# Kernel optimization log

Hardware: AMD Instinct MI355X
Metric: run time of the kernel (lower is better)

## Reference

```python
import jax, jax.numpy as jnp
import numpy as np

B, DIM, HEADS, HEAD_DIM = 4, 768, 8, 96
THW = (8, 28, 28)
N_TOK = THW[0] * THW[1] * THW[2] + 1  # +1 cls token = 6273
HIDDEN = 4 * DIM
STRIDE = (1, 2, 2)
SCALE = HEAD_DIM ** -0.5


def layernorm(x, w, b, eps=1e-5):
    mu = x.mean(-1, keepdims=True)
    var = ((x - mu) ** 2).mean(-1, keepdims=True)
    return (x - mu) / jnp.sqrt(var + eps) * w + b


def conv_pool(x, w):
    # depthwise 3D conv: x [BN, C, T, H, W], w [C, 1, 3, 3, 3], stride (1,2,2), pad 1
    return jax.lax.conv_general_dilated(
        x, w, window_strides=STRIDE, padding=[(1, 1), (1, 1), (1, 1)],
        dimension_numbers=('NCDHW', 'OIDHW', 'NCDHW'),
        feature_group_count=x.shape[1])


def attn_pool(x, conv_w, norm_w, norm_b):
    # x: [B, h, N, d]; pool spatial tokens (excluding cls), then LayerNorm(head_dim)
    cls, xs = x[:, :, :1], x[:, :, 1:]
    b, h, _, d = xs.shape
    t, hh, ww = THW
    xs = xs.reshape(b * h, t, hh, ww, d).transpose(0, 4, 1, 2, 3)  # [bh, d, t, h, w]
    xs = conv_pool(xs, conv_w)
    l_pooled = xs.shape[2] * xs.shape[3] * xs.shape[4]
    xs = xs.reshape(b, h, d, l_pooled).transpose(0, 1, 3, 2)  # [B, h, L, d]
    xs = jnp.concatenate([cls, xs], axis=2)
    return layernorm(xs, norm_w, norm_b)


def max_pool_skip(x):
    # residual-path MaxPool3d: kernel (1,3,3), stride (1,2,2), pad (0,1,1); cls excluded
    cls, xs = x[:, :1], x[:, 1:]
    b, _, c = xs.shape
    t, hh, ww = THW
    xs = xs.reshape(b, t, hh, ww, c)
    xs = jax.lax.reduce_window(
        xs, -jnp.inf, jax.lax.max,
        (1, 1, 3, 3, 1), (1, 1, 2, 2, 1),
        [(0, 0), (0, 0), (1, 1), (1, 1), (0, 0)])
    xs = xs.reshape(b, -1, c)
    return jnp.concatenate([cls, xs], axis=1)


def setup_inputs() -> dict:
    key = jax.random.key(0)
    ks = jax.random.split(key, 16)
    s = 0.02
    inp = {
        'x': jax.random.normal(ks[0], (B, N_TOK, DIM), jnp.float32),
        'n1_w': jnp.ones((DIM,), jnp.float32), 'n1_b': jnp.zeros((DIM,), jnp.float32),
        'wq': jax.random.normal(ks[1], (DIM, DIM), jnp.float32) * s,
        'bq': jnp.zeros((DIM,), jnp.float32),
        'wk': jax.random.normal(ks[2], (DIM, DIM), jnp.float32) * s,
        'bk': jnp.zeros((DIM,), jnp.float32),
        'wv': jax.random.normal(ks[3], (DIM, DIM), jnp.float32) * s,
        'bv': jnp.zeros((DIM,), jnp.float32),
        'pq_w': jax.random.normal(ks[4], (HEAD_DIM, 1, 3, 3, 3), jnp.float32) * s,
        'pk_w': jax.random.normal(ks[5], (HEAD_DIM, 1, 3, 3, 3), jnp.float32) * s,
        'pv_w': jax.random.normal(ks[6], (HEAD_DIM, 1, 3, 3, 3), jnp.float32) * s,
        'nq_w': jnp.ones((HEAD_DIM,), jnp.float32), 'nq_b': jnp.zeros((HEAD_DIM,), jnp.float32),
        'nk_w': jnp.ones((HEAD_DIM,), jnp.float32), 'nk_b': jnp.zeros((HEAD_DIM,), jnp.float32),
        'nv_w': jnp.ones((HEAD_DIM,), jnp.float32), 'nv_b': jnp.zeros((HEAD_DIM,), jnp.float32),
        'proj_w': jax.random.normal(ks[7], (DIM, DIM), jnp.float32) * s,
        'proj_b': jnp.zeros((DIM,), jnp.float32),
        'n2_w': jnp.ones((DIM,), jnp.float32), 'n2_b': jnp.zeros((DIM,), jnp.float32),
        'fc1_w': jax.random.normal(ks[8], (HIDDEN, DIM), jnp.float32) * s,
        'fc1_b': jnp.zeros((HIDDEN,), jnp.float32),
        'fc2_w': jax.random.normal(ks[9], (DIM, HIDDEN), jnp.float32) * s,
        'fc2_b': jnp.zeros((DIM,), jnp.float32),
    }
    return inp


def reference(x, n1_w, n1_b, wq, bq, wk, bk, wv, bv, pq_w, pk_w, pv_w,
              nq_w, nq_b, nk_w, nk_b, nv_w, nv_b, proj_w, proj_b,
              n2_w, n2_b, fc1_w, fc1_b, fc2_w, fc2_b):
    b, n, _ = x.shape
    xn = layernorm(x, n1_w, n1_b)
    # q/k/v projections -> [B, h, N, d]
    q = (xn @ wq.T + bq).reshape(b, n, HEADS, HEAD_DIM).transpose(0, 2, 1, 3)
    k = (xn @ wk.T + bk).reshape(b, n, HEADS, HEAD_DIM).transpose(0, 2, 1, 3)
    v = (xn @ wv.T + bv).reshape(b, n, HEADS, HEAD_DIM).transpose(0, 2, 1, 3)
    q = attn_pool(q, pq_w, nq_w, nq_b)
    k = attn_pool(k, pk_w, nk_w, nk_b)
    v = attn_pool(v, pv_w, nv_w, nv_b)
    attn = jax.nn.softmax(jnp.einsum('bhqd,bhkd->bhqk', q, k) * SCALE, axis=-1)
    o = jnp.einsum('bhqk,bhkd->bhqd', attn, v)
    nq = o.shape[2]
    o = o.transpose(0, 2, 1, 3).reshape(b, nq, DIM)
    o = o @ proj_w.T + proj_b
    # residual with pooled skip
    x2 = max_pool_skip(x) + o
    xn2 = layernorm(x2, n2_w, n2_b)
    m = jax.nn.gelu(xn2 @ fc1_w.T + fc1_b, approximate=False) @ fc2_w.T + fc2_b
    return x2 + m
```

## Files before the change

kernel.cpp:

```cpp
#include <hip/hip_runtime.h>
#include <math.h>

#define B_ 4
#define NTOK 6273
#define DIMD 768
#define HEADS 8
#define HD 96
#define NPOOL 1569
#define NPAD 1600
#define HID 3072
#define MROWS (B_*NTOK)
#define M2 (B_*NPOOL)
#define SCALE_ 0.10206207261596575f

typedef float f32x4 __attribute__((ext_vector_type(4)));
typedef short s16x8 __attribute__((ext_vector_type(8)));
typedef short s16x4 __attribute__((ext_vector_type(4)));
typedef unsigned u32x3 __attribute__((ext_vector_type(3)));

__device__ __forceinline__ short f2bf(float f){
  unsigned u = __builtin_bit_cast(unsigned, f);
  u = (u + 0x7fffu + ((u >> 16) & 1u)) >> 16;
  return (short)u;
}
__device__ __forceinline__ float bf2f(short s){
  unsigned u = ((unsigned)(unsigned short)s) << 16;
  return __builtin_bit_cast(float, u);
}
__device__ __forceinline__ float bfsel(unsigned u, int hi){
  unsigned r = hi ? (u & 0xffff0000u) : (u << 16);
  return __builtin_bit_cast(float, r);
}
__device__ __forceinline__ unsigned pack2(float lo, float hi){
  return (unsigned)(unsigned short)f2bf(lo) | ((unsigned)(unsigned short)f2bf(hi) << 16);
}

__device__ __forceinline__ void gld16(const void* g, void* l){
  __builtin_amdgcn_global_load_lds((const __attribute__((address_space(1))) unsigned*)g,
                                   (__attribute__((address_space(3))) unsigned*)l, 16, 0, 0);
}

#if defined(__has_builtin)
#if __has_builtin(__builtin_amdgcn_mfma_f32_16x16x16bf16_1k)
#define MFMA16K(a,b,c) __builtin_amdgcn_mfma_f32_16x16x16bf16_1k(a,b,c,0,0,0)
#endif
#endif
#ifndef MFMA16K
__device__ __forceinline__ f32x4 mfma16k_asm(s16x4 a, s16x4 b, f32x4 c){
  asm volatile("v_mfma_f32_16x16x16_bf16 %0, %1, %2, %0\n\ts_nop 7\n\ts_nop 7"
               : "+v"(c) : "v"(a), "v"(b));
  return c;
}
#define MFMA16K(a,b,c) mfma16k_asm(a,b,c)
#endif

template<int NT>
__device__ __forceinline__ float block_sum(float v, float* red){
  int t = threadIdx.x;
  red[t] = v; __syncthreads();
  #pragma unroll
  for (int s = NT/2; s > 0; s >>= 1){
    if (t < s) red[t] += red[t+s];
    __syncthreads();
  }
  float r = red[0];
  __syncthreads();
  return r;
}

__device__ __forceinline__ unsigned xcd_serial(unsigned bid, unsigned nwg){
  unsigned q = nwg >> 3, r8 = nwg & 7;
  unsigned xcd = bid & 7, idx = bid >> 3;
  return (xcd < r8 ? xcd*(q+1) : r8*(q+1) + (xcd-r8)*q) + idx;
}

template<int STR, int STC>
__device__ __forceinline__ void tile_decode(unsigned serial, int& rowT, int& colT){
  const int nStC = (int)gridDim.x / STC;
  int st = (int)serial / (STR*STC);
  int t  = (int)serial - st*(STR*STC);
  int stR = st / nStC, stC = st - stR*nStC;
  int c = t / STR, r = t - c*STR;
  rowT = stR*STR + r;
  colT = stC*STC + c;
}

__global__ void castw(const float* s0,const float* s1,const float* s2,const float* s3,
                      const float* s4,const float* s5,
                      short* d0,short* d1,short* d2,short* d3,short* d4,short* d5){
  const float* s; short* d; int n;
  switch(blockIdx.y){
    case 0: s=s0; d=d0; n=589824; break;
    case 1: s=s1; d=d1; n=589824; break;
    case 2: s=s2; d=d2; n=589824; break;
    case 3: s=s3; d=d3; n=589824; break;
    case 4: s=s4; d=d4; n=2359296; break;
    default: s=s5; d=d5; n=2359296; break;
  }
  for (int i = blockIdx.x*blockDim.x + threadIdx.x; i < n; i += gridDim.x*blockDim.x)
    d[i] = f2bf(s[i]);
}

__global__ __launch_bounds__(256) void packb(const float* b0, const float* b1, const float* b2, float* o){
  int i = blockIdx.x*256 + threadIdx.x;
  if (i < 768) o[i] = b0[i];
  else if (i < 1536) o[i] = b1[i-768];
  else if (i < 2304) o[i] = b2[i-1536];
}

__global__ __launch_bounds__(256) void ln768(const float* __restrict__ x, const float* __restrict__ w,
                      const float* __restrict__ b, short* __restrict__ out){
  int row = blockIdx.x*4 + (threadIdx.x >> 6);
  int lane = threadIdx.x & 63;
  const float* xr = x + (size_t)row*DIMD + lane*12;
  f32x4 v0 = *(const f32x4*)(xr);
  f32x4 v1 = *(const f32x4*)(xr + 4);
  f32x4 v2 = *(const f32x4*)(xr + 8);
  float v[12] = { v0[0],v0[1],v0[2],v0[3], v1[0],v1[1],v1[2],v1[3], v2[0],v2[1],v2[2],v2[3] };
  float s = 0.f;
  #pragma unroll
  for (int j=0;j<12;j++) s += v[j];
  #pragma unroll
  for (int m=1; m<64; m<<=1) s += __shfl_xor(s, m);
  float mu = s * (1.f/768.f);
  float sq = 0.f;
  #pragma unroll
  for (int j=0;j<12;j++){ float d = v[j]-mu; sq += d*d; }
  #pragma unroll
  for (int m=1; m<64; m<<=1) sq += __shfl_xor(sq, m);
  float rstd = rsqrtf(sq*(1.f/768.f) + 1e-5f);
  int c0 = lane*12;
  float o[12];
  #pragma unroll
  for (int j=0;j<12;j++) o[j] = (v[j]-mu)*rstd*w[c0+j] + b[c0+j];
  unsigned* po = (unsigned*)(out + (size_t)row*DIMD + c0);
  #pragma unroll
  for (int k=0;k<6;k++) po[k] = pack2(o[2*k], o[2*k+1]);
}

__global__ __launch_bounds__(512) void gemm8(const short* __restrict__ A, const short* __restrict__ Bw,
                        const float* __restrict__ bias, short* __restrict__ Cb,
                        int M, int N, int K){
  __shared__ short lds[4][16384];
  int tid = threadIdx.x;
  int w = tid >> 6, lane = tid & 63;
  int l15 = lane & 15, g = (lane >> 4) & 3;
  int wr = w >> 2, wc = w & 3;

  unsigned nwg = gridDim.x * gridDim.y;
  unsigned bid = blockIdx.y * gridDim.x + blockIdx.x;
  unsigned serial = bid;
  if (nwg >= 512) serial = xcd_serial(bid, nwg);
  int rowBase = (int)(serial / gridDim.x) * 256;
  int colBase = (int)(serial % gridDim.x) * 256;

  const short* pa[2]; const short* pb[2];
  #pragma unroll
  for (int j=0;j<2;j++){
    int mr = rowBase + (w + j*8)*16 + l15; if (mr >= M) mr = M-1;
    int nr = colBase + (w + j*8)*16 + l15;
    pa[j] = A  + (size_t)mr*K + g*8;
    pb[j] = Bw + (size_t)nr*K + g*8;
  }
  int sd = tid*8;

  auto stage = [&](int slot, int p){
    int koff = p*32;
    short* base = &lds[slot][0];
    #pragma unroll
    for (int j=0;j<2;j++){
      gld16(pa[j] + koff, base + sd + j*4096);
      gld16(pb[j] + koff, base + 8192 + sd + j*4096);
    }
  };

  f32x4 acc[8][4] = {};
  int np = K >> 5;
  stage(0, 0);
  if (np > 1) stage(1, 1);
  if (np > 2) stage(2, 2);
  for (int p = 0; p < np; p++){
    if (p <= np-3)
      asm volatile("s_waitcnt vmcnt(8)" ::: "memory");
    else if (p == np-2)
      asm volatile("s_waitcnt vmcnt(4)" ::: "memory");
    else
      asm volatile("s_waitcnt vmcnt(0)" ::: "memory");
    __builtin_amdgcn_s_barrier();
    if (p + 3 < np) stage((p+3)&3, p+3);
    const short* lA = &lds[p&3][0];
    const short* lB = lA + 8192;
    s16x8 bfr[4];
    #pragma unroll
    for (int nf=0; nf<4; nf++)
      bfr[nf] = *(const s16x8*)(lB + (wc*4+nf)*512 + lane*8);
    __builtin_amdgcn_s_setprio(1);
    #pragma unroll
    for (int mf=0; mf<8; mf++){
      s16x8 af = *(const s16x8*)(lA + (wr*8+mf)*512 + lane*8);
      #pragma unroll
      for (int nf=0; nf<4; nf++)
        acc[mf][nf] = __builtin_amdgcn_mfma_f32_16x16x32_bf16(af, bfr[nf], acc[mf][nf], 0,0,0);
    }
    __builtin_amdgcn_s_setprio(0);
  }

  __syncthreads();
  short* ldsC = &lds[0][0];
  #pragma unroll
  for (int mf=0; mf<8; mf++){
    int rowL0 = wr*128 + mf*16 + g*4;
    #pragma unroll
    for (int nf=0; nf<4; nf++){
      int colL = wc*64 + nf*16 + l15;
      float bv = bias[colBase + colL];
      int ch = colL >> 3, in8 = colL & 7;
      #pragma unroll
      for (int r=0;r<4;r++){
        int rL = rowL0 + r;
        int chs = ch ^ ((rL >> 2) & 7);
        ldsC[rL*256 + chs*8 + in8] = f2bf(acc[mf][nf][r] + bv);
      }
    }
  }
  __syncthreads();
  int ch2 = tid & 31, rg = tid >> 5;
  #pragma unroll
  for (int i=0;i<16;i++){
    int rowL = rg + i*16;
    int chs = ch2 ^ ((rowL >> 2) & 7);
    s16x8 v = *(const s16x8*)(ldsC + rowL*256 + chs*8);
    int rr = rowBase + rowL;
    if (rr < M) *(s16x8*)(Cb + (size_t)rr*N + colBase + ch2*8) = v;
  }
}

template<int GELU, int OUTBF16, int RESID, int STR, int STC>
__global__ __launch_bounds__(256) void gemm_bt(const short* __restrict__ A, const short* __restrict__ Bw,
                        const float* __restrict__ bias, const float* __restrict__ resid,
                        float* __restrict__ Cf, short* __restrict__ Cb,
                        int M, int N, int K){
  __shared__ short lds[3][8192];
  int tid = threadIdx.x;
  int lane = tid & 63, wv = tid >> 6;
  int wr = wv >> 1, wc = wv & 1;
  int l15 = lane & 15, g = lane >> 4;

  unsigned nwg = gridDim.x * gridDim.y;
  unsigned bid = blockIdx.y * gridDim.x + blockIdx.x;
  unsigned serial = xcd_serial(bid, nwg);
  int rowT, colT;
  tile_decode<STR,STC>(serial, rowT, colT);
  int rowBase = rowT * 128;
  int colBase = colT * 128;

  f32x4 acc[4][4] = {};
  int srow = (tid & 15) | ((tid >> 6) << 4);
  int scol = ((tid >> 4) & 3) * 8;
  int ldsoff = tid * 8;

  int ar0 = rowBase + srow;      if (ar0 >= M) ar0 = M-1;
  int ar1 = rowBase + srow + 64; if (ar1 >= M) ar1 = M-1;
  int br0 = colBase + srow;
  const short* pa0 = A  + (size_t)ar0*K + scol;
  const short* pa1 = A  + (size_t)ar1*K + scol;
  const short* pb0 = Bw + (size_t)br0*K + scol;
  const short* pb1 = Bw + (size_t)(br0+64)*K + scol;

  auto stage = [&](int s, int kt){
    gld16(pa0 + kt, &lds[s][ldsoff]);
    gld16(pa1 + kt, &lds[s][ldsoff + 2048]);
    gld16(pb0 + kt, &lds[s][4096 + ldsoff]);
    gld16(pb1 + kt, &lds[s][4096 + ldsoff + 2048]);
  };

  int nk = K >> 5;
  stage(0, 0);
  if (nk > 1) stage(1, 32);
  for (int kt = 0; kt < nk; kt++){
    int cur = kt % 3;
    if (kt + 2 < nk){
      stage((kt+2)%3, (kt+2)*32);
      asm volatile("s_waitcnt vmcnt(8)" ::: "memory");
    } else if (kt + 1 < nk){
      asm volatile("s_waitcnt vmcnt(4)" ::: "memory");
    } else {
      asm volatile("s_waitcnt vmcnt(0)" ::: "memory");
    }
    __builtin_amdgcn_s_barrier();
    const short* la = lds[cur];
    const short* lb = lds[cur] + 4096;
    s16x8 af[4], bfr[4];
    #pragma unroll
    for (int m=0;m<4;m++) af[m]  = *(const s16x8*)(la + (wr*4 + m)*512 + g*128 + l15*8);
    #pragma unroll
    for (int n=0;n<4;n++) bfr[n] = *(const s16x8*)(lb + (wc*4 + n)*512 + g*128 + l15*8);
    #pragma unroll
    for (int m=0;m<4;m++)
      #pragma unroll
      for (int n=0;n<4;n++)
        acc[m][n] = __builtin_amdgcn_mfma_f32_16x16x32_bf16(af[m], bfr[n], acc[m][n], 0,0,0);
    __builtin_amdgcn_s_barrier();
  }

  if (OUTBF16){
    short* ldsC = &lds[0][0];
    #pragma unroll
    for (int n=0;n<4;n++){
      int colL = wc*64 + n*16 + l15;
      float bv = bias[colBase + colL];
      #pragma unroll
      for (int m=0;m<4;m++){
        #pragma unroll
        for (int r=0;r<4;r++){
          int rowL = wr*64 + m*16 + g*4 + r;
          float v = acc[m][n][r] + bv;
          if (GELU) v = 0.5f*v*(1.f + erff(v*0.70710678118654752f));
          int ch = colL >> 3, in8 = colL & 7;
          int chs = ch ^ (((rowL >> 2) & 3) << 2);
          ldsC[rowL*128 + chs*8 + in8] = f2bf(v);
        }
      }
    }
    __syncthreads();
    int ch = tid & 15, rg = tid >> 4;
    #pragma unroll
    for (int i=0;i<8;i++){
      int rowL = rg + i*16;
      int chs = ch ^ (((rowL >> 2) & 3) << 2);
      s16x8 v = *(const s16x8*)(ldsC + rowL*128 + chs*8);
      int rr = rowBase + rowL;
      if (rr < M) *(s16x8*)(Cb + (size_t)rr*N + colBase + ch*8) = v;
    }
  } else {
    #pragma unroll
    for (int m=0;m<4;m++){
      int row = rowBase + wr*64 + m*16 + g*4;
      #pragma unroll
      for (int n=0;n<4;n++){
        int col = colBase + wc*64 + n*16 + l15;
        float bv = bias[col];
        #pragma unroll
        for (int r=0;r<4;r++){
          int rr = row + r;
          if (rr < M){
            float v = acc[m][n][r] + bv;
            if (GELU) v = 0.5f*v*(1.f + erff(v*0.70710678118654752f));
            if (RESID) v += resid[(size_t)rr*N + col];
            Cf[(size_t)rr*N + col] = v;
          }
        }
      }
    }
  }
}

template<int RESID>
__global__ __launch_bounds__(256) void gemm_n64(const short* __restrict__ A, const short* __restrict__ Bw,
                        const float* __restrict__ bias, const float* __restrict__ resid,
                        float* __restrict__ Cf, int M, int N, int K){
  __shared__ short lds[3][6144];
  int tid = threadIdx.x;
  int lane = tid & 63, wc = tid >> 6;
  int l15 = lane & 15, g = lane >> 4;

  unsigned nwg = gridDim.x * gridDim.y;
  unsigned bid = blockIdx.y * gridDim.x + blockIdx.x;
  unsigned serial = xcd_serial(bid, nwg);
  int rowBase = (int)(serial / gridDim.x) * 64;
  int colBase = (int)(serial % gridDim.x) * 128;

  f32x4 acc[4][2] = {};
  int srow = (tid & 15) | ((tid >> 6) << 4);
  int scol = ((tid >> 4) & 3) * 8;
  int ldsoff = tid * 8;

  int ar = rowBase + srow; if (ar >= M) ar = M-1;
  int br = colBase + srow;
  const short* pa  = A  + (size_t)ar*K + scol;
  const short* pb0 = Bw + (size_t)br*K + scol;
  const short* pb1 = Bw + (size_t)(br+64)*K + scol;

  auto stage = [&](int s, int kt){
    gld16(pa  + kt, &lds[s][ldsoff]);
    gld16(pb0 + kt, &lds[s][2048 + ldsoff]);
    gld16(pb1 + kt, &lds[s][4096 + ldsoff]);
  };

  int nk = K >> 5;
  stage(0, 0);
  if (nk > 1) stage(1, 32);
  for (int kt = 0; kt < nk; kt++){
    int cur = kt % 3;
    if (kt + 2 < nk){
      stage((kt+2)%3, (kt+2)*32);
      asm volatile("s_waitcnt vmcnt(6)" ::: "memory");
    } else if (kt + 1 < nk){
      asm volatile("s_waitcnt vmcnt(3)" ::: "memory");
    } else {
      asm volatile("s_waitcnt vmcnt(0)" ::: "memory");
    }
    __builtin_amdgcn_s_barrier();
    const short* la = lds[cur];
    const short* lb = lds[cur] + 2048;
    s16x8 af[4], bfr[2];
    #pragma unroll
    for (int m=0;m<4;m++) af[m]  = *(const s16x8*)(la + m*512 + g*128 + l15*8);
    #pragma unroll
    for (int n=0;n<2;n++) bfr[n] = *(const s16x8*)(lb + (wc*2 + n)*512 + g*128 + l15*8);
    #pragma unroll
    for (int m=0;m<4;m++)
      #pragma unroll
      for (int n=0;n<2;n++)
        acc[m][n] = __builtin_amdgcn_mfma_f32_16x16x32_bf16(af[m], bfr[n], acc[m][n], 0,0,0);
    __builtin_amdgcn_s_barrier();
  }
  #pragma unroll
  for (int m=0;m<4;m++){
    int row = rowBase + m*16 + g*4;
    #pragma unroll
    for (int n=0;n<2;n++){
      int col = colBase + wc*32 + n*16 + l15;
      float bv = bias[col];
      #pragma unroll
      for (int r=0;r<4;r++){
        int rr = row + r;
        if (rr < M){
          float v = acc[m][n][r] + bv;
          if (RESID) v += resid[(size_t)rr*N + col];
          Cf[(size_t)rr*N + col] = v;
        }
      }
    }
  }
}

__global__ __launch_bounds__(256, 2) void pool_conv3(
    const short* __restrict__ raw,
    const float* __restrict__ cwq, const float* __restrict__ cwk, const float* __restrict__ cwv,
    const float* __restrict__ nqw, const float* __restrict__ nqb,
    const float* __restrict__ nkw, const float* __restrict__ nkb,
    const float* __restrict__ nvw, const float* __restrict__ nvb,
    short* __restrict__ qo, short* __restrict__ ko, short* __restrict__ vo){
  unsigned nwg = gridDim.x * gridDim.y * gridDim.z;
  unsigned lin = (blockIdx.z*gridDim.y + blockIdx.y)*gridDim.x + blockIdx.x;
  unsigned serial = xcd_serial(lin, nwg);
  int ho = (int)(serial % 14);
  unsigned rest = serial / 14;
  int bh = (int)(rest & 31);
  int z  = (int)(rest >> 5);
  int t = threadIdx.x;
  int g = t >> 4;
  if (g >= 14) return;
  int s = t & 15, d = s*6;
  const float* cw = (z==0) ? cwq : (z==1) ? cwk : cwv;
  const float* nw = (z==0) ? nqw : (z==1) ? nkw : nvw;
  const float* nb = (z==0) ? nqb : (z==1) ? nkb : nvb;
  const short* base = raw + (size_t)(bh>>3)*NTOK*2304 + z*768 + (bh&7)*96 + d;
  float acc[8][6] = {};
  #pragma unroll
  for (int dh=0; dh<3; dh++){
    int ih = 2*ho - 1 + dh;
    if (ih < 0 || ih >= 28) continue;
    #pragma unroll
    for (int dw=0; dw<3; dw++){
      int iw = 2*g - 1 + dw;
      if (iw < 0 || iw >= 28) continue;
      float w[3][6];
      #pragma unroll
      for (int dt=0; dt<3; dt++)
        #pragma unroll
        for (int j=0;j<6;j++)
          w[dt][j] = cw[(d+j)*27 + dt*9 + dh*3 + dw];
      #pragma unroll
      for (int it=0; it<8; it++){
        u32x3 u = *(const u32x3*)(base + (size_t)(1 + (it*28+ih)*28 + iw)*2304);
        float in[6] = { bfsel(u[0],0), bfsel(u[0],1), bfsel(u[1],0),
                        bfsel(u[1],1), bfsel(u[2],0), bfsel(u[2],1) };
        #pragma unroll
        for (int dt=0; dt<3; dt++){
          int to = it + 1 - dt;
          if (to < 0 || to > 7) continue;
          #pragma unroll
          for (int j=0;j<6;j++) acc[to][j] = fmaf(in[j], w[dt][j], acc[to][j]);
        }
      }
    }
  }
  float nwv[6], nbv[6];
  #pragma unroll
  for (int j=0;j<6;j++){ nwv[j] = nw[d+j]; nbv[j] = nb[d+j]; }
  #pragma unroll
  for (int to=0; to<8; to++){
    float sm = acc[to][0]+acc[to][1]+acc[to][2]+acc[to][3]+acc[to][4]+acc[to][5];
    #pragma unroll
    for (int m=1; m<16; m<<=1) sm += __shfl_xor(sm, m);
    float mu = sm*(1.f/96.f);
    float vr = 0.f;
    #pragma unroll
    for (int j=0;j<6;j++){ float dd = acc[to][j]-mu; vr += dd*dd; }
    #pragma unroll
    for (int m=1; m<16; m<<=1) vr += __shfl_xor(vr, m);
    float rstd = rsqrtf(vr*(1.f/96.f) + 1e-5f);
    int tok = 1 + to*196 + ho*14 + g;
    if (z == 0){
      short o[6];
      #pragma unroll
      for (int j=0;j<6;j++) o[j] = f2bf((acc[to][j]-mu)*rstd*nwv[j] + nbv[j]);
      unsigned* q32 = (unsigned*)(qo + ((size_t)bh*NPAD + tok)*96 + d);
      #pragma unroll
      for (int w2=0; w2<3; w2++)
        q32[w2] = (unsigned)(unsigned short)o[2*w2] | ((unsigned)(unsigned short)o[2*w2+1] << 16);
    } else if (z == 1){
      size_t kb = (size_t)bh*NPAD*96 + (size_t)(tok>>4)*1536 + (tok&15)*8;
      #pragma unroll
      for (int j=0;j<6;j++){
        int dj = d + j;
        ko[kb + (dj>>5)*512 + ((dj>>3)&3)*128 + (dj&7)] = f2bf((acc[to][j]-mu)*rstd*nwv[j] + nbv[j]);
      }
    } else {
      size_t vb = (size_t)bh*NPAD*96 + (size_t)(tok>>6)*6144 + ((tok>>4)&3)*256 + ((tok>>2)&3)*64 + (tok&3);
      #pragma unroll
      for (int j=0;j<6;j++){
        int dj = d + j;
        vo[vb + (dj>>4)*1024 + (dj&15)*4] = f2bf((acc[to][j]-mu)*rstd*nwv[j] + nbv[j]);
      }
    }
  }
}

__global__ __launch_bounds__(128) void cls3(
    const short* __restrict__ raw,
    const float* __restrict__ nqw, const float* __restrict__ nqb,
    const float* __restrict__ nkw, const float* __restrict__ nkb,
    const float* __restrict__ nvw, const float* __restrict__ nvb,
    short* __restrict__ qo, short* __restrict__ ko, short* __restrict__ vo){
  int b = blockIdx.x, t = threadIdx.x;
  int h = t >> 4, s = t & 15, d = s*6;
  int bh = b*8 + h;
  const float* nws[3] = { nqw, nkw, nvw };
  const float* nbs[3] = { nqb, nkb, nvb };
  #pragma unroll
  for (int ten=0; ten<3; ten++){
    const short* row = raw + (size_t)b*NTOK*2304 + ten*768 + h*96 + d;
    u32x3 u = *(const u32x3*)(row);
    float a[6] = { bfsel(u[0],0), bfsel(u[0],1), bfsel(u[1],0), bfsel(u[1],1), bfsel(u[2],0), bfsel(u[2],1) };
    float sm = a[0]+a[1]+a[2]+a[3]+a[4]+a[5];
    #pragma unroll
    for (int m=1; m<16; m<<=1) sm += __shfl_xor(sm, m);
    float mu = sm*(1.f/96.f);
    float vr2 = 0.f;
    #pragma unroll
    for (int j=0;j<6;j++){ float dd = a[j]-mu; vr2 += dd*dd; }
    #pragma unroll
    for (int m=1; m<16; m<<=1) vr2 += __shfl_xor(vr2, m);
    float rstd = rsqrtf(vr2*(1.f/96.f) + 1e-5f);
    #pragma unroll
    for (int j=0;j<6;j++){
      int dj = d + j;
      short o = f2bf((a[j]-mu)*rstd*nws[ten][dj] + nbs[ten][dj]);
      if (ten == 0)      qo[((size_t)bh*NPAD)*96 + dj] = o;
      else if (ten == 1) ko[(size_t)bh*NPAD*96 + (dj>>5)*512 + ((dj>>3)&3)*128 + (dj&7)] = o;
      else               vo[(size_t)bh*NPAD*96 + (dj>>4)*1024 + (dj&15)*4] = o;
    }
  }
}

__global__ __launch_bounds__(96) void padfill(short* __restrict__ qo, short* __restrict__ ko, short* __restrict__ vo){
  int tok = NPOOL + blockIdx.x;
  int bh = blockIdx.y;
  int d = threadIdx.x;
  qo[((size_t)bh*NPAD + tok)*96 + d] = 0;
  size_t kb = (size_t)bh*NPAD*96 + (size_t)(tok>>4)*1536 + (tok&15)*8;
  ko[kb + (d>>5)*512 + ((d>>3)&3)*128 + (d&7)] = 0;
  size_t vb = (size_t)bh*NPAD*96 + (size_t)(tok>>6)*6144 + ((tok>>4)&3)*256 + ((tok>>2)&3)*64 + (tok&3);
  vo[vb + (d>>4)*1024 + (d&15)*4] = 0;
}

__global__ __launch_bounds__(512) void attn_k(const short* __restrict__ qp, const short* __restrict__ kp,
                       const short* __restrict__ vp, short* __restrict__ oattn){
  const float M0 = 6.0f;
  __shared__ short lkv[2][12288];
  unsigned nwg = gridDim.x * gridDim.y;
  unsigned bid0 = blockIdx.y * gridDim.x + blockIdx.x;
  unsigned serial = xcd_serial(bid0, nwg);
  int bh = (int)(serial / 13);
  int qblk = (int)(serial - (unsigned)bh*13);
  int b = bh >> 3, h = bh & 7;
  int tid = threadIdx.x;
  int lane = tid & 63, wv = tid >> 6;
  int l15 = lane & 15, g = lane >> 4;
  int qi = qblk*128 + wv*16 + l15;
  int qi_ld = qi < NPAD ? qi : NPAD-1;
  const short* qbase = qp + (size_t)bh*NPAD*HD;
  const short* kbase = kp + (size_t)bh*NPAD*HD;
  const short* vbase = vp + (size_t)bh*NPAD*HD;
  s16x8 qf[3];
  #pragma unroll
  for (int f=0; f<3; f++)
    qf[f] = *(const s16x8*)(qbase + (size_t)qi_ld*HD + f*32 + g*8);

  auto stage = [&](int bsel, int t){
    #pragma unroll
    for (int i=0;i<3;i++){
      int off = i*4096 + tid*8;
      const short* src = (off < 6144) ? (kbase + t*6144 + off) : (vbase + t*6144 + off - 6144);
      gld16(src, &lkv[bsel][off]);
    }
  };

  f32x4 accO[6] = {};
  float tsum = 0.f;

  stage(0, 0);
  asm volatile("s_waitcnt vmcnt(0)" ::: "memory");
  __builtin_amdgcn_s_barrier();

  for (int kt = 0; kt < 25; kt++){
    int cur = kt & 1;
    if (kt < 24){
      stage(cur^1, kt+1);
      asm volatile("s_waitcnt vmcnt(3)" ::: "memory");
    } else {
      asm volatile("s_waitcnt vmcnt(0)" ::: "memory");
    }
    __builtin_amdgcn_s_barrier();

    const short* lkc = &lkv[cur][0];
    const short* lvc = &lkv[cur][6144];
    f32x4 sacc[4];
    #pragma unroll
    for (int sub=0; sub<4; sub++){
      sacc[sub] = (f32x4){0.f,0.f,0.f,0.f};
      #pragma unroll
      for (int f=0; f<3; f++){
        s16x8 kf = *(const s16x8*)(lkc + sub*1536 + f*512 + lane*8);
        sacc[sub] = __builtin_amdgcn_mfma_f32_16x16x32_bf16(kf, qf[f], sacc[sub], 0,0,0);
      }
    }
    s16x4 pf[4];
    if (kt < 24){
      #pragma unroll
      for (int sub=0; sub<4; sub++){
        #pragma unroll
        for (int r=0; r<4; r++){
          float p = __expf(sacc[sub][r]*SCALE_ - M0);
          tsum += p;
          pf[sub][r] = f2bf(p);
        }
      }
    } else {
      #pragma unroll
      for (int sub=0; sub<4; sub++){
        #pragma unroll
        for (int r=0; r<4; r++){
          int ki = kt*64 + sub*16 + g*4 + r;
          float p = (ki < NPOOL) ? __expf(sacc[sub][r]*SCALE_ - M0) : 0.f;
          tsum += p;
          pf[sub][r] = f2bf(p);
        }
      }
    }
    #pragma unroll
    for (int dt=0; dt<6; dt++){
      #pragma unroll
      for (int sub=0; sub<4; sub++){
        s16x4 vf = *(const s16x4*)(lvc + dt*1024 + sub*256 + lane*4);
        accO[dt] = MFMA16K(vf, pf[sub], accO[dt]);
      }
    }
    __builtin_amdgcn_s_barrier();
  }

  tsum += __shfl_xor(tsum, 16);
  tsum += __shfl_xor(tsum, 32);
  if (qi < NPOOL){
    float inv = 1.f / tsum;
    #pragma unroll
    for (int dt=0; dt<6; dt++){
      #pragma unroll
      for (int r=0; r<4; r++){
        int dd = dt*16 + g*4 + r;
        oattn[((size_t)b*NPOOL + qi)*DIMD + h*96 + dd] = f2bf(accO[dt][r] * inv);
      }
    }
  }
}

__global__ __launch_bounds__(256) void skip_ln2(const float* __restrict__ x, const float* __restrict__ oproj,
                         const float* __restrict__ w, const float* __restrict__ bb,
                         float* __restrict__ x2, short* __restrict__ xn2){
  unsigned nwg = gridDim.x * gridDim.y;
  unsigned bid = blockIdx.y * gridDim.x + blockIdx.x;
  unsigned serial = xcd_serial(bid, nwg);
  int b = (int)(serial / NPOOL);
  int tok = (int)(serial - (unsigned)b*NPOOL);
  int t = threadIdx.x;
  __shared__ float red[256];
  float v[3];
  int ot = tok - 1;
  int to = ot/196, rem = ot%196, ho = rem/14, wo = rem%14;
  #pragma unroll
  for (int i=0;i<3;i++){
    int c = t + i*256;
    float mv;
    if (tok == 0){
      mv = x[(size_t)b*NTOK*DIMD + c];
    } else {
      mv = -INFINITY;
      #pragma unroll
      for (int dh=0; dh<3; dh++){
        int ih = 2*ho - 1 + dh; if (ih < 0 || ih >= 28) continue;
        #pragma unroll
        for (int dw=0; dw<3; dw++){
          int iw = 2*wo - 1 + dw; if (iw < 0 || iw >= 28) continue;
          int n = 1 + (to*28 + ih)*28 + iw;
          mv = fmaxf(mv, x[((size_t)b*NTOK + n)*DIMD + c]);
        }
      }
    }
    float val = mv + oproj[((size_t)b*NPOOL + tok)*DIMD + c];
    x2[((size_t)b*NPOOL + tok)*DIMD + c] = val;
    v[i] = val;
  }
  float s = v[0]+v[1]+v[2];
  s = block_sum<256>(s, red);
  float mu = s * (1.f/768.f);
  float sq = 0.f;
  #pragma unroll
  for (int i=0;i<3;i++){ float d = v[i]-mu; sq += d*d; }
  sq = block_sum<256>(sq, red);
  float rstd = rsqrtf(sq*(1.f/768.f) + 1e-5f);
  #pragma unroll
  for (int i=0;i<3;i++){
    int c = t + i*256;
    xn2[((size_t)b*NPOOL + tok)*DIMD + c] = f2bf((v[i]-mu)*rstd*w[c] + bb[c]);
  }
}

extern "C" void kernel_launch(void* const* d_in, const int* in_sizes, int n_in,
                              void* d_out, int out_size, void* d_ws, size_t ws_size,
                              hipStream_t stream){
  (void)in_sizes; (void)n_in; (void)out_size; (void)ws_size;
  const float* x      = (const float*)d_in[0];
  const float* n1_w   = (const float*)d_in[1];
  const float* n1_b   = (const float*)d_in[2];
  const float* wq     = (const float*)d_in[3];
  const float* bq     = (const float*)d_in[4];
  const float* wk     = (const float*)d_in[5];
  const float* bk     = (const float*)d_in[6];
  const float* wv     = (const float*)d_in[7];
  const float* bv     = (const float*)d_in[8];
  const float* pq_w   = (const float*)d_in[9];
  const float* pk_w   = (const float*)d_in[10];
  const float* pv_w   = (const float*)d_in[11];
  const float* nq_w   = (const float*)d_in[12];
  const float* nq_b   = (const float*)d_in[13];
  const float* nk_w   = (const float*)d_in[14];
  const float* nk_b   = (const float*)d_in[15];
  const float* nv_w   = (const float*)d_in[16];
  const float* nv_b   = (const float*)d_in[17];
  const float* proj_w = (const float*)d_in[18];
  const float* proj_b = (const float*)d_in[19];
  const float* n2_w   = (const float*)d_in[20];
  const float* n2_b   = (const float*)d_in[21];
  const float* fc1_w  = (const float*)d_in[22];
  const float* fc1_b  = (const float*)d_in[23];
  const float* fc2_w  = (const float*)d_in[24];
  const float* fc2_b  = (const float*)d_in[25];
  float* out = (float*)d_out;

  char* ws = (char*)d_ws;
  size_t off = 0;
  auto take = [&](size_t bytes)->char*{
    char* p = ws + off; off = (off + bytes + 255) & ~(size_t)255; return p;
  };
  short* xn  = (short*)take(38541312);
  short* wqb = (short*)take(1179648);
  short* wkb = (short*)take(1179648);
  short* wvb = (short*)take(1179648);
  short* wpb = (short*)take(1179648);
  short* w1b = (short*)take(4718592);
  short* w2b = (short*)take(4718592);
  float* bcat= (float*)take(9216);
  char*  big = take(115623936);
  short* qkv  = (short*)(big);
  short* oattn= (short*)(big);
  float* oproj= (float*)(big + 9639936);
  float* x2   = (float*)(big + 28919808);
  short* xn2  = (short*)(big + 48199680);
  short* h1   = (short*)(big + 57839616);
  short* qp   = (short*)take(9830400);
  short* kp   = (short*)take(9830400);
  short* vT   = (short*)take(9830400);

  castw<<<dim3(2304,6), 256, 0, stream>>>(wq,wk,wv,proj_w,fc1_w,fc2_w, wqb,wkb,wvb,wpb,w1b,w2b);
  packb<<<9, 256, 0, stream>>>(bq, bk, bv, bcat);
  ln768<<<6273, 256, 0, stream>>>(x, n1_w, n1_b, xn);

  gemm8<<<dim3(9,99), 512, 0, stream>>>(xn, wqb, bcat, qkv, MROWS, 2304, 768);

  pool_conv3<<<dim3(32,14,3), 256, 0, stream>>>(qkv, pq_w, pk_w, pv_w,
                                                nq_w, nq_b, nk_w, nk_b, nv_w, nv_b, qp, kp, vT);
  cls3<<<dim3(B_), 128, 0, stream>>>(qkv, nq_w, nq_b, nk_w, nk_b, nv_w, nv_b, qp, kp, vT);
  padfill<<<dim3(31,32), 96, 0, stream>>>(qp, kp, vT);

  attn_k<<<dim3(13,32), 512, 0, stream>>>(qp, kp, vT, oattn);

  gemm_n64<0><<<dim3(6,99), 256, 0, stream>>>(oattn, wpb, proj_b, nullptr, oproj, M2, 768, 768);

  skip_ln2<<<dim3(NPOOL,B_), 256, 0, stream>>>(x, oproj, n2_w, n2_b, x2, xn2);

  gemm_bt<1,1,0,10,8><<<dim3(24,50), 256, 0, stream>>>(xn2, w1b, fc1_b, nullptr, nullptr, h1, M2, HID, 768);
  gemm_n64<1><<<dim3(6,99), 256, 0, stream>>>(h1, w2b, fc2_b, x2, out, M2, 768, 3072);
}
```

Baseline: 599.6 us.

## Fuse small prologue/pooling kernels and use wave-level LayerNorm in skip path

Merges weight casting, bias packing and the first LayerNorm into one prologue kernel. The cls-token normalization and pad zero-fill are folded into extra blocks of the pooling kernel. skip_ln2 is rewritten to handle one token per wavefront, using vectorized loads and shuffle reductions in place of a block-wide shared-memory reduction. This removes several launches and the syncthreads-heavy reduction, but the prologue's strided weight-cast loop may be less efficient than the dedicated cast kernel.

Result: faster. 571.2 us (-4.7%).

```diff
diff --git a/kernel.cpp b/kernel.cpp
--- a/kernel.cpp
+++ b/kernel.cpp
@@ -54,20 +54,6 @@
 #define MFMA16K(a,b,c) mfma16k_asm(a,b,c)
 #endif
 
-template<int NT>
-__device__ __forceinline__ float block_sum(float v, float* red){
-  int t = threadIdx.x;
-  red[t] = v; __syncthreads();
-  #pragma unroll
-  for (int s = NT/2; s > 0; s >>= 1){
-    if (t < s) red[t] += red[t+s];
-    __syncthreads();
-  }
-  float r = red[0];
-  __syncthreads();
-  return r;
-}
-
 __device__ __forceinline__ unsigned xcd_serial(unsigned bid, unsigned nwg){
   unsigned q = nwg >> 3, r8 = nwg & 7;
   unsigned xcd = bid & 7, idx = bid >> 3;
@@ -85,57 +71,58 @@
   colT = stC*STC + c;
 }
 
-__global__ void castw(const float* s0,const float* s1,const float* s2,const float* s3,
-                      const float* s4,const float* s5,
-                      short* d0,short* d1,short* d2,short* d3,short* d4,short* d5){
-  const float* s; short* d; int n;
-  switch(blockIdx.y){
-    case 0: s=s0; d=d0; n=589824; break;
-    case 1: s=s1; d=d1; n=589824; break;
-    case 2: s=s2; d=d2; n=589824; break;
-    case 3: s=s3; d=d3; n=589824; break;
-    case 4: s=s4; d=d4; n=2359296; break;
-    default: s=s5; d=d5; n=2359296; break;
-  }
-  for (int i = blockIdx.x*blockDim.x + threadIdx.x; i < n; i += gridDim.x*blockDim.x)
-    d[i] = f2bf(s[i]);
-}
-
-__global__ __launch_bounds__(256) void packb(const float* b0, const float* b1, const float* b2, float* o){
-  int i = blockIdx.x*256 + threadIdx.x;
-  if (i < 768) o[i] = b0[i];
-  else if (i < 1536) o[i] = b1[i-768];
-  else if (i < 2304) o[i] = b2[i-1536];
-}
-
-__global__ __launch_bounds__(256) void ln768(const float* __restrict__ x, const float* __restrict__ w,
-                      const float* __restrict__ b, short* __restrict__ out){
-  int row = blockIdx.x*4 + (threadIdx.x >> 6);
-  int lane = threadIdx.x & 63;
-  const float* xr = x + (size_t)row*DIMD + lane*12;
-  f32x4 v0 = *(const f32x4*)(xr);
-  f32x4 v1 = *(const f32x4*)(xr + 4);
-  f32x4 v2 = *(const f32x4*)(xr + 8);
-  float v[12] = { v0[0],v0[1],v0[2],v0[3], v1[0],v1[1],v1[2],v1[3], v2[0],v2[1],v2[2],v2[3] };
-  float s = 0.f;
-  #pragma unroll
-  for (int j=0;j<12;j++) s += v[j];
-  #pragma unroll
-  for (int m=1; m<64; m<<=1) s += __shfl_xor(s, m);
-  float mu = s * (1.f/768.f);
-  float sq = 0.f;
-  #pragma unroll
-  for (int j=0;j<12;j++){ float d = v[j]-mu; sq += d*d; }
-  #pragma unroll
-  for (int m=1; m<64; m<<=1) sq += __shfl_xor(sq, m);
-  float rstd = rsqrtf(sq*(1.f/768.f) + 1e-5f);
-  int c0 = lane*12;
-  float o[12];
-  #pragma unroll
-  for (int j=0;j<12;j++) o[j] = (v[j]-mu)*rstd*w[c0+j] + b[c0+j];
-  unsigned* po = (unsigned*)(out + (size_t)row*DIMD + c0);
-  #pragma unroll
-  for (int k=0;k<6;k++) po[k] = pack2(o[2*k], o[2*k+1]);
+__global__ __launch_bounds__(256) void prologue(
+    const float* __restrict__ x, const float* __restrict__ n1w, const float* __restrict__ n1b,
+    short* __restrict__ xn,
+    const float* __restrict__ wq, const float* __restrict__ wk, const float* __restrict__ wv,
+    const float* __restrict__ wp, const float* __restrict__ w1, const float* __restrict__ w2,
+    short* __restrict__ wqb, short* __restrict__ wkb, short* __restrict__ wvb,
+    short* __restrict__ wpb, short* __restrict__ w1b, short* __restrict__ w2b,
+    const float* __restrict__ bq, const float* __restrict__ bk, const float* __restrict__ bv,
+    float* __restrict__ bcat){
+  if (blockIdx.y == 0){
+    int row = blockIdx.x*4 + (threadIdx.x >> 6);
+    int lane = threadIdx.x & 63;
+    const float* xr = x + (size_t)row*DIMD + lane*12;
+    f32x4 v0 = *(const f32x4*)(xr);
+    f32x4 v1 = *(const f32x4*)(xr + 4);
+    f32x4 v2 = *(const f32x4*)(xr + 8);
+    float v[12] = { v0[0],v0[1],v0[2],v0[3], v1[0],v1[1],v1[2],v1[3], v2[0],v2[1],v2[2],v2[3] };
+    float s = 0.f;
+    #pragma unroll
+    for (int j=0;j<12;j++) s += v[j];
+    #pragma unroll
+    for (int m=1; m<64; m<<=1) s += __shfl_xor(s, m);
+    float mu = s * (1.f/768.f);
+    float sq = 0.f;
+    #pragma unroll
+    for (int j=0;j<12;j++){ float d = v[j]-mu; sq += d*d; }
+    #pragma unroll
+    for (int m=1; m<64; m<<=1) sq += __shfl_xor(sq, m);
+    float rstd = rsqrtf(sq*(1.f/768.f) + 1e-5f);
+    int c0 = lane*12;
+    float o[12];
+    #pragma unroll
+    for (int j=0;j<12;j++) o[j] = (v[j]-mu)*rstd*n1w[c0+j] + n1b[c0+j];
+    unsigned* po = (unsigned*)(xn + (size_t)row*DIMD + c0);
+    #pragma unroll
+    for (int k=0;k<6;k++) po[k] = pack2(o[2*k], o[2*k+1]);
+  } else {
+    unsigned gid = blockIdx.x*256u + threadIdx.x;
+    if (gid < 768u) bcat[gid] = bq[gid];
+    else if (gid < 1536u) bcat[gid] = bk[gid-768u];
+    else if (gid < 2304u) bcat[gid] = bv[gid-1536u];
+    for (unsigned i = gid; i < 7077888u; i += 6273u*256u){
+      const float* s; short* d; unsigned off;
+      if (i < 2359296u){
+        unsigned r = i / 589824u; off = i - r*589824u;
+        s = (r==0)?wq:(r==1)?wk:(r==2)?wv:wp;
+        d = (r==0)?wqb:(r==1)?wkb:(r==2)?wvb:wpb;
+      } else if (i < 4718592u){ off = i - 2359296u; s = w1; d = w1b; }
+      else                    { off = i - 4718592u; s = w2; d = w2b; }
+      d[off] = f2bf(s[off]);
+    }
+  }
 }
 
 __global__ __launch_bounds__(512) void gemm8(const short* __restrict__ A, const short* __restrict__ Bw,
@@ -445,17 +432,58 @@
   unsigned nwg = gridDim.x * gridDim.y * gridDim.z;
   unsigned lin = (blockIdx.z*gridDim.y + blockIdx.y)*gridDim.x + blockIdx.x;
   unsigned serial = xcd_serial(lin, nwg);
-  int ho = (int)(serial % 14);
-  unsigned rest = serial / 14;
+  int ho = (int)(serial % 15);
+  unsigned rest = serial / 15;
   int bh = (int)(rest & 31);
   int z  = (int)(rest >> 5);
   int t = threadIdx.x;
+  const float* nw = (z==0) ? nqw : (z==1) ? nkw : nvw;
+  const float* nb = (z==0) ? nqb : (z==1) ? nkb : nvb;
+
+  if (ho == 14){
+    if (t < 16){
+      int s2 = t, d2 = s2*6;
+      const short* row = raw + (size_t)(bh>>3)*NTOK*2304 + z*768 + (bh&7)*96 + d2;
+      u32x3 u = *(const u32x3*)(row);
+      float a[6] = { bfsel(u[0],0), bfsel(u[0],1), bfsel(u[1],0), bfsel(u[1],1), bfsel(u[2],0), bfsel(u[2],1) };
+      float sm = a[0]+a[1]+a[2]+a[3]+a[4]+a[5];
+      #pragma unroll
+      for (int m=1; m<16; m<<=1) sm += __shfl_xor(sm, m);
+      float mu = sm*(1.f/96.f);
+      float vr2 = 0.f;
+      #pragma unroll
+      for (int j=0;j<6;j++){ float dd = a[j]-mu; vr2 += dd*dd; }
+      #pragma unroll
+      for (int m=1; m<16; m<<=1) vr2 += __shfl_xor(vr2, m);
+      float rstd = rsqrtf(vr2*(1.f/96.f) + 1e-5f);
+      #pragma unroll
+      for (int j=0;j<6;j++){
+        int dj = d2 + j;
+        short o = f2bf((a[j]-mu)*rstd*nw[dj] + nb[dj]);
+        if (z == 0)      qo[((size_t)bh*NPAD)*96 + dj] = o;
+        else if (z == 1) ko[(size_t)bh*NPAD*96 + (dj>>5)*512 + ((dj>>3)&3)*128 + (dj&7)] = o;
+        else             vo[(size_t)bh*NPAD*96 + (dj>>4)*1024 + (dj&15)*4] = o;
+      }
+    }
+    for (int i = t; i < 31*96; i += 256){
+      int tok = NPOOL + i/96;
+      int dd = i - (i/96)*96;
+      if (z == 0) qo[((size_t)bh*NPAD + tok)*96 + dd] = 0;
+      else if (z == 1){
+        size_t kb = (size_t)bh*NPAD*96 + (size_t)(tok>>4)*1536 + (tok&15)*8;
+        ko[kb + (dd>>5)*512 + ((dd>>3)&3)*128 + (dd&7)] = 0;
+      } else {
+        size_t vb = (size_t)bh*NPAD*96 + (size_t)(tok>>6)*6144 + ((tok>>4)&3)*256 + ((tok>>2)&3)*64 + (tok&3);
+        vo[vb + (dd>>4)*1024 + (dd&15)*4] = 0;
+      }
+    }
+    return;
+  }
+
   int g = t >> 4;
   if (g >= 14) return;
   int s = t & 15, d = s*6;
   const float* cw = (z==0) ? cwq : (z==1) ? cwk : cwv;
-  const float* nw = (z==0) ? nqw : (z==1) ? nkw : nvw;
-  const float* nb = (z==0) ? nqb : (z==1) ? nkb : nvb;
   const short* base = raw + (size_t)(bh>>3)*NTOK*2304 + z*768 + (bh&7)*96 + d;
   float acc[8][6] = {};
   #pragma unroll
@@ -527,54 +555,6 @@
       }
     }
   }
-}
-
-__global__ __launch_bounds__(128) void cls3(
-    const short* __restrict__ raw,
-    const float* __restrict__ nqw, const float* __restrict__ nqb,
-    const float* __restrict__ nkw, const float* __restrict__ nkb,
-    const float* __restrict__ nvw, const float* __restrict__ nvb,
-    short* __restrict__ qo, short* __restrict__ ko, short* __restrict__ vo){
-  int b = blockIdx.x, t = threadIdx.x;
-  int h = t >> 4, s = t & 15, d = s*6;
-  int bh = b*8 + h;
-  const float* nws[3] = { nqw, nkw, nvw };
-  const float* nbs[3] = { nqb, nkb, nvb };
-  #pragma unroll
-  for (int ten=0; ten<3; ten++){
-    const short* row = raw + (size_t)b*NTOK*2304 + ten*768 + h*96 + d;
-    u32x3 u = *(const u32x3*)(row);
-    float a[6] = { bfsel(u[0],0), bfsel(u[0],1), bfsel(u[1],0), bfsel(u[1],1), bfsel(u[2],0), bfsel(u[2],1) };
-    float sm = a[0]+a[1]+a[2]+a[3]+a[4]+a[5];
-    #pragma unroll
-    for (int m=1; m<16; m<<=1) sm += __shfl_xor(sm, m);
-    float mu = sm*(1.f/96.f);
-    float vr2 = 0.f;
-    #pragma unroll
-    for (int j=0;j<6;j++){ float dd = a[j]-mu; vr2 += dd*dd; }
-    #pragma unroll
-    for (int m=1; m<16; m<<=1) vr2 += __shfl_xor(vr2, m);
-    float rstd = rsqrtf(vr2*(1.f/96.f) + 1e-5f);
-    #pragma unroll
-    for (int j=0;j<6;j++){
-      int dj = d + j;
-      short o = f2bf((a[j]-mu)*rstd*nws[ten][dj] + nbs[ten][dj]);
-      if (ten == 0)      qo[((size_t)bh*NPAD)*96 + dj] = o;
-      else if (ten == 1) ko[(size_t)bh*NPAD*96 + (dj>>5)*512 + ((dj>>3)&3)*128 + (dj&7)] = o;
-      else               vo[(size_t)bh*NPAD*96 + (dj>>4)*1024 + (dj&15)*4] = o;
-    }
-  }
-}
-
-__global__ __launch_bounds__(96) void padfill(short* __restrict__ qo, short* __restrict__ ko, short* __restrict__ vo){
-  int tok = NPOOL + blockIdx.x;
-  int bh = blockIdx.y;
-  int d = threadIdx.x;
-  qo[((size_t)bh*NPAD + tok)*96 + d] = 0;
-  size_t kb = (size_t)bh*NPAD*96 + (size_t)(tok>>4)*1536 + (tok&15)*8;
-  ko[kb + (d>>5)*512 + ((d>>3)&3)*128 + (d&7)] = 0;
-  size_t vb = (size_t)bh*NPAD*96 + (size_t)(tok>>6)*6144 + ((tok>>4)&3)*256 + ((tok>>2)&3)*64 + (tok&3);
-  vo[vb + (d>>4)*1024 + (d&15)*4] = 0;
 }
 
 __global__ __launch_bounds__(512) void attn_k(const short* __restrict__ qp, const short* __restrict__ kp,
@@ -690,52 +670,65 @@
 __global__ __launch_bounds__(256) void skip_ln2(const float* __restrict__ x, const float* __restrict__ oproj,
                          const float* __restrict__ w, const float* __restrict__ bb,
                          float* __restrict__ x2, short* __restrict__ xn2){
-  unsigned nwg = gridDim.x * gridDim.y;
-  unsigned bid = blockIdx.y * gridDim.x + blockIdx.x;
-  unsigned serial = xcd_serial(bid, nwg);
-  int b = (int)(serial / NPOOL);
-  int tok = (int)(serial - (unsigned)b*NPOOL);
-  int t = threadIdx.x;
-  __shared__ float red[256];
-  float v[3];
-  int ot = tok - 1;
-  int to = ot/196, rem = ot%196, ho = rem/14, wo = rem%14;
-  #pragma unroll
-  for (int i=0;i<3;i++){
-    int c = t + i*256;
-    float mv;
-    if (tok == 0){
-      mv = x[(size_t)b*NTOK*DIMD + c];
-    } else {
-      mv = -INFINITY;
-      #pragma unroll
-      for (int dh=0; dh<3; dh++){
-        int ih = 2*ho - 1 + dh; if (ih < 0 || ih >= 28) continue;
+  unsigned serial = xcd_serial(blockIdx.x, gridDim.x);
+  int ti = (int)serial*4 + (int)(threadIdx.x >> 6);
+  int b = ti / NPOOL;
+  int tok = ti - b*NPOOL;
+  int lane = threadIdx.x & 63;
+  int c0 = lane*12;
+  float v[12];
+  if (tok == 0){
+    const float* xr = x + (size_t)b*NTOK*DIMD + c0;
+    f32x4 a0 = *(const f32x4*)xr, a1 = *(const f32x4*)(xr+4), a2 = *(const f32x4*)(xr+8);
+    #pragma unroll
+    for (int j=0;j<4;j++){ v[j]=a0[j]; v[4+j]=a1[j]; v[8+j]=a2[j]; }
+  } else {
+    int ot = tok - 1;
+    int to = ot/196, rem = ot%196, ho = rem/14, wo = rem%14;
+    #pragma unroll
+    for (int j=0;j<12;j++) v[j] = -INFINITY;
+    #pragma unroll
+    for (int dh=0; dh<3; dh++){
+      int ih = 2*ho - 1 + dh; if (ih < 0 || ih >= 28) continue;
+      #pragma unroll
+      for (int dw=0; dw<3; dw++){
+        int iw = 2*wo - 1 + dw; if (iw < 0 || iw >= 28) continue;
+        const float* xr = x + ((size_t)b*NTOK + 1 + (to*28 + ih)*28 + iw)*DIMD + c0;
+        f32x4 a0 = *(const f32x4*)xr, a1 = *(const f32x4*)(xr+4), a2 = *(const f32x4*)(xr+8);
         #pragma unroll
-        for (int dw=0; dw<3; dw++){
-          int iw = 2*wo - 1 + dw; if (iw < 0 || iw >= 28) continue;
-          int n = 1 + (to*28 + ih)*28 + iw;
-          mv = fmaxf(mv, x[((size_t)b*NTOK + n)*DIMD + c]);
+        for (int j=0;j<4;j++){
+          v[j]   = fmaxf(v[j],   a0[j]);
+          v[4+j] = fmaxf(v[4+j], a1[j]);
+          v[8+j] = fmaxf(v[8+j], a2[j]);
         }
       }
     }
-    float val = mv + oproj[((size_t)b*NPOOL + tok)*DIMD + c];
-    x2[((size_t)b*NPOOL + tok)*DIMD + c] = val;
-    v[i] = val;
-  }
-  float s = v[0]+v[1]+v[2];
-  s = block_sum<256>(s, red);
+  }
+  const float* opr = oproj + ((size_t)b*NPOOL + tok)*DIMD + c0;
+  f32x4 p0 = *(const f32x4*)opr, p1 = *(const f32x4*)(opr+4), p2 = *(const f32x4*)(opr+8);
+  #pragma unroll
+  for (int j=0;j<4;j++){ v[j]+=p0[j]; v[4+j]+=p1[j]; v[8+j]+=p2[j]; }
+  float* x2r = x2 + ((size_t)b*NPOOL + tok)*DIMD + c0;
+  f32x4 o0 = {v[0],v[1],v[2],v[3]}, o1 = {v[4],v[5],v[6],v[7]}, o2 = {v[8],v[9],v[10],v[11]};
+  *(f32x4*)x2r = o0; *(f32x4*)(x2r+4) = o1; *(f32x4*)(x2r+8) = o2;
+  float s = 0.f;
+  #pragma unroll
+  for (int j=0;j<12;j++) s += v[j];
+  #pragma unroll
+  for (int m=1; m<64; m<<=1) s += __shfl_xor(s, m);
   float mu = s * (1.f/768.f);
   float sq = 0.f;
   #pragma unroll
-  for (int i=0;i<3;i++){ float d = v[i]-mu; sq += d*d; }
-  sq = block_sum<256>(sq, red);
+  for (int j=0;j<12;j++){ float d = v[j]-mu; sq += d*d; }
+  #pragma unroll
+  for (int m=1; m<64; m<<=1) sq += __shfl_xor(sq, m);
   float rstd = rsqrtf(sq*(1.f/768.f) + 1e-5f);
-  #pragma unroll
-  for (int i=0;i<3;i++){
-    int c = t + i*256;
-    xn2[((size_t)b*NPOOL + tok)*DIMD + c] = f2bf((v[i]-mu)*rstd*w[c] + bb[c]);
-  }
+  float o[12];
+  #pragma unroll
+  for (int j=0;j<12;j++) o[j] = (v[j]-mu)*rstd*w[c0+j] + bb[c0+j];
+  unsigned* po = (unsigned*)(xn2 + ((size_t)b*NPOOL + tok)*DIMD + c0);
+  #pragma unroll
+  for (int k=0;k<6;k++) po[k] = pack2(o[2*k], o[2*k+1]);
 }
 
 extern "C" void kernel_launch(void* const* d_in, const int* in_sizes, int n_in,
@@ -794,22 +787,20 @@
   short* kp   = (short*)take(9830400);
   short* vT   = (short*)take(9830400);
 
-  castw<<<dim3(2304,6), 256, 0, stream>>>(wq,wk,wv,proj_w,fc1_w,fc2_w, wqb,wkb,wvb,wpb,w1b,w2b);
-  packb<<<9, 256, 0, stream>>>(bq, bk, bv, bcat);
-  ln768<<<6273, 256, 0, stream>>>(x, n1_w, n1_b, xn);
+  prologue<<<dim3(6273,2), 256, 0, stream>>>(x, n1_w, n1_b, xn,
+      wq, wk, wv, proj_w, fc1_w, fc2_w, wqb, wkb, wvb, wpb, w1b, w2b,
+      bq, bk, bv, bcat);
 
   gemm8<<<dim3(9,99), 512, 0, stream>>>(xn, wqb, bcat, qkv, MROWS, 2304, 768);
 
-  pool_conv3<<<dim3(32,14,3), 256, 0, stream>>>(qkv, pq_w, pk_w, pv_w,
+  pool_conv3<<<dim3(32,15,3), 256, 0, stream>>>(qkv, pq_w, pk_w, pv_w,
                                                 nq_w, nq_b, nk_w, nk_b, nv_w, nv_b, qp, kp, vT);
-  cls3<<<dim3(B_), 128, 0, stream>>>(qkv, nq_w, nq_b, nk_w, nk_b, nv_w, nv_b, qp, kp, vT);
-  padfill<<<dim3(31,32), 96, 0, stream>>>(qp, kp, vT);
 
   attn_k<<<dim3(13,32), 512, 0, stream>>>(qp, kp, vT, oattn);
 
   gemm_n64<0><<<dim3(6,99), 256, 0, stream>>>(oattn, wpb, proj_b, nullptr, oproj, M2, 768, 768);
 
-  skip_ln2<<<dim3(NPOOL,B_), 256, 0, stream>>>(x, oproj, n2_w, n2_b, x2, xn2);
+  skip_ln2<<<1569, 256, 0, stream>>>(x, oproj, n2_w, n2_b, x2, xn2);
 
   gemm_bt<1,1,0,10,8><<<dim3(24,50), 256, 0, stream>>>(xn2, w1b, fc1_b, nullptr, nullptr, h1, M2, HID, 768);
   gemm_n64<1><<<dim3(6,99), 256, 0, stream>>>(h1, w2b, fc2_b, x2, out, M2, 768, 3072);
```
